# Kernel optimization log

Hardware: AMD Instinct MI355X
Metric: run time of the kernel (lower is better)

Reference implementation:

```python
import jax, jax.numpy as jnp
import numpy as np


def _dequantize_int4(qweight, scales, qzeros, blocksize):
    """Unpack int4 weights (two nibbles per byte along N) and dequantize.

    qweight: [K, N/2] int (byte values 0..255); low nibble = even col, high nibble = odd col
    scales:  [groups, N] float32, groups = K // blocksize
    qzeros:  [groups, N/2] int (packed like qweight)
    returns: [K, N] float32 dequantized weight, w = (q - z) * s per group along K
    """
    K, Nh = qweight.shape
    N = Nh * 2
    groups = scales.shape[0]
    low = (qweight & 0xF).astype(jnp.float32)
    high = ((qweight >> 4) & 0xF).astype(jnp.float32)
    wq = jnp.stack([low, high], axis=-1).reshape(K, N)  # [K, N]
    zl = (qzeros & 0xF).astype(jnp.float32)
    zh = ((qzeros >> 4) & 0xF).astype(jnp.float32)
    zq = jnp.stack([zl, zh], axis=-1).reshape(groups, N)  # [groups, N]
    # group-wise dequant along K without materializing repeated scale/zero tables
    w = (wq.reshape(groups, blocksize, N) - zq[:, None, :]) * scales[:, None, :]
    return w.reshape(K, N)


def setup_inputs() -> dict:
    key = jax.random.key(0)
    k1, k2, k3, k4, k5 = jax.random.split(key, 5)
    B, S, K = 32, 64, 4096
    N_PAD = 32064
    BLOCKSIZE = 128
    GROUPS = K // BLOCKSIZE
    x = jax.random.normal(k1, (B, S, K), dtype=jnp.float32)
    qweight = jax.random.randint(k2, (K, N_PAD // 2), 0, 256, dtype=jnp.int32)
    scales = jax.random.uniform(k3, (GROUPS, N_PAD), dtype=jnp.float32) * 0.02 + 1e-3
    qzeros = jax.random.randint(k4, (GROUPS, N_PAD // 2), 0, 256, dtype=jnp.int32)
    bias = jax.random.normal(k5, (N_PAD,), dtype=jnp.float32) * 0.01
    return {"x": x, "qweight": qweight, "scales": scales, "qzeros": qzeros,
            "bias": bias, "blocksize": BLOCKSIZE, "n_dim": 32000}


def reference(x, qweight, scales, qzeros, bias, blocksize, n_dim):
    # mimic module.forward with acc_test=False: keep only the last token
    if x.ndim > 3:
        x = x.reshape(-1, x.shape[-2], x.shape[-1])
    x_last = x[:, -1:, :]  # [B, 1, K]
    w = _dequantize_int4(qweight, scales, qzeros, blocksize)  # [K, N_pad]
    out = jnp.einsum('bsk,kn->bsn', x_last, w) + bias  # mm_bias_int4
    return out[:, :, :n_dim]  # strip vocab padding
```

## Files before the change

kernel.cpp:

```cpp
#include <hip/hip_runtime.h>
#include <hip/hip_bf16.h>


typedef _Float16 f16x8 __attribute__((ext_vector_type(8)));
typedef _Float16 f16x2 __attribute__((ext_vector_type(2)));
typedef float f32x4 __attribute__((ext_vector_type(4)));
typedef int i32x2 __attribute__((ext_vector_type(2)));

#define K_DIM 4096
#define NP 16032
#define NSC 32064
#define NOUT 32000
#define S_LEN 64
#define QROWB ((size_t)NP * 4)
#define QSTEP (32u * (uint32_t)NP * 4u)

__global__ void prep_a_kernel(const float* __restrict__ x,
                              _Float16* __restrict__ aws) {
    int tid = blockIdx.x * 256 + threadIdx.x;
    int m = tid >> 9;
    int q = tid & 511;
    const float* xp = x + ((size_t)m * S_LEN + (S_LEN - 1)) * K_DIM + q * 8;
    f32x4 u0 = *(const f32x4*)xp;
    f32x4 u1 = *(const f32x4*)(xp + 4);
    int ks = q >> 2;
    int h = q & 3;
    int mblk = m >> 4;
    f16x8 d;
#pragma unroll
    for (int j = 0; j < 4; ++j) {
        d[j] = (_Float16)u0[j];
        d[4 + j] = (_Float16)u1[j];
    }
    *(f16x8*)(aws + ((size_t)((ks * 2 + mblk) * 64 + h * 16 + (m & 15))) * 8) = d;
}

__global__ __launch_bounds__(512, 4)
void q4gemm_kernel(const int* __restrict__ qw,
                   const float* __restrict__ scales,
                   const int* __restrict__ qzeros,
                   const float* __restrict__ bias,
                   const _Float16* __restrict__ aws,
                   float* __restrict__ out) {
    __shared__ float red[8 * 2048];

    const int tid = threadIdx.x;
    const int w = tid >> 6;
    const int l = tid & 63;
    const int h = l >> 4;
    const int c = l & 15;
    const int n0 = blockIdx.x * 64;
    const int np0 = n0 >> 1;

    const char* qwb = (const char*)qw;
    uint32_t qoff = (uint32_t)((w * 512 + 8 * h) * (size_t)NP + np0 + 2 * c) * 4u;

    f32x4 acc0[4] = {};
    f32x4 acc1[4] = {};
    f16x2 vz[4], vs[4];
    f32x4 gsc;
    i32x2 gzw;
    i32x2 qa[8], qb[8];
    f16x8 afa0, afa1, afb0, afb1;

#define QLD(buf)                                                              \
    do {                                                                      \
        _Pragma("unroll") for (int j = 0; j < 8; ++j)                         \
            buf[j] = *(const i32x2*)(qwb + qoff + (size_t)j * QROWB);         \
        qoff += QSTEP;                                                        \
    } while (0)

#define GRP_LOAD(g)                                                           \
    do {                                                                      \
        int gg = (g) > 31 ? 31 : (g);                                         \
        gsc = *(const f32x4*)(scales + (size_t)gg * NSC + n0 + 4 * c);        \
        gzw = *(const i32x2*)(qzeros + (size_t)gg * NP + np0 + 2 * c);        \
    } while (0)

#define GRP_EXPAND()                                                          \
    do {                                                                      \
        _Pragma("unroll") for (int s = 0; s < 4; ++s) {                       \
            const int bs = s >> 1, o = s & 1;                                 \
            int zn = (gzw[bs] >> (4 * o)) & 15;                               \
            int z16 = 0x6400 | (o ? (zn << 4) : zn);                          \
            int zp = z16 | (z16 << 16);                                       \
            vz[s] = __builtin_bit_cast(f16x2, zp);                            \
            float sf = gsc[s] * (o ? 0.0625f : 1.0f);                         \
            _Float16 hf = (_Float16)sf;                                       \
            f16x2 sp = {hf, hf};                                              \
            vs[s] = sp;                                                       \
        }                                                                     \
    } while (0)

#define ALD(A0, A1, tloc)                                                     \
    do {                                                                      \
        int ksg_ = w * 16 + (tloc);                                           \
        A0 = *(const f16x8*)(aws + ((size_t)(ksg_ * 2 + 0) * 64 + l) * 8);    \
        A1 = *(const f16x8*)(aws + ((size_t)(ksg_ * 2 + 1) * 64 + l) * 8);    \
    } while (0)

#define COMPUTE(buf, A0, A1)                                                  \
    do {                                                                      \
        _Pragma("unroll") for (int bs = 0; bs < 2; ++bs) {                    \
            int tc[4];                                                        \
            _Pragma("unroll") for (int p = 0; p < 4; ++p)                     \
                tc[p] = (buf[2 * p + 1][bs] << 16) | buf[2 * p][bs];          \
            _Pragma("unroll") for (int o = 0; o < 2; ++o) {                   \
                const int s = 2 * bs + o;                                     \
                const int msk = o ? 0x00F000F0 : 0x000F000F;                  \
                int4 bi;                                                      \
                _Pragma("unroll") for (int p = 0; p < 4; ++p) {               \
                    int vqi = (tc[p] & msk) | 0x64006400;                     \
                    f16x2 vq = __builtin_bit_cast(f16x2, vqi);                \
                    f16x2 r = (vq - vz[s]) * vs[s];                           \
                    bi[p] = __builtin_bit_cast(int, r);                       \
                }                                                             \
                f16x8 b = __builtin_bit_cast(f16x8, bi);                      \
                acc0[s] = __builtin_amdgcn_mfma_f32_16x16x32_f16(A0, b, acc0[s], 0, 0, 0); \
                acc1[s] = __builtin_amdgcn_mfma_f32_16x16x32_f16(A1, b, acc1[s], 0, 0, 0); \
            }                                                                 \
        }                                                                     \
    } while (0)

    QLD(qa);
    GRP_LOAD(w * 4);
    GRP_EXPAND();
    GRP_LOAD(w * 4 + 1);
    ALD(afa0, afa1, 0);

#pragma unroll
    for (int tt = 0; tt < 8; ++tt) {
        QLD(qb);
        ALD(afb0, afb1, 2 * tt + 1);
        if (tt != 0 && (tt & 1) == 0) {
            GRP_EXPAND();
            GRP_LOAD(w * 4 + tt / 2 + 1);
        }
        COMPUTE(qa, afa0, afa1);
        if (tt < 7) {
            QLD(qa);
            ALD(afa0, afa1, 2 * tt + 2);
        }
        COMPUTE(qb, afb0, afb1);
    }

#pragma unroll
    for (int s = 0; s < 4; ++s)
#pragma unroll
        for (int r = 0; r < 4; ++r) {
            red[w * 2048 + (h * 4 + r) * 64 + 4 * c + s] = acc0[s][r];
            red[w * 2048 + (16 + h * 4 + r) * 64 + 4 * c + s] = acc1[s][r];
        }

    __syncthreads();

#pragma unroll
    for (int i = 0; i < 4; ++i) {
        int e = i * 512 + tid;
        float sum = 0.f;
#pragma unroll
        for (int ww = 0; ww < 8; ++ww) sum += red[ww * 2048 + e];
        int m = e >> 6;
        int n = n0 + (e & 63);
        out[(size_t)m * NOUT + n] = sum + bias[n];
    }
}

extern "C" void kernel_launch(void* const* d_in, const int* in_sizes, int n_in,
                              void* d_out, int out_size, void* d_ws, size_t ws_size,
                              hipStream_t stream) {
    const float* x       = (const float*)d_in[0];
    const int*   qweight = (const int*)d_in[1];
    const float* scales  = (const float*)d_in[2];
    const int*   qzeros  = (const int*)d_in[3];
    const float* bias    = (const float*)d_in[4];

    _Float16* aws = (_Float16*)d_ws;
    float* out = (float*)d_out;

    prep_a_kernel<<<64, 256, 0, stream>>>(x, aws);
    q4gemm_kernel<<<500, 512, 0, stream>>>(qweight, scales, qzeros, bias, aws, out);
}
```

Baseline: 50.47 us.

## Widen GEMM tile to 128 columns per block with 16-byte weight loads

Each block now covers 128 output columns instead of 64. Each lane loads 16-byte qweight/qzeros vectors and handles 8 column subsets, which doubles the accumulators per thread. The cross-wave reduction is split into two passes through the same shared buffer, one for each M half, with an extra barrier between them. This halves the grid to 250 blocks and lowers the occupancy hint to 2 blocks per CU, trading parallelism and register pressure for wider memory transactions and less per-block overhead.

```diff
diff --git a/kernel.cpp b/kernel.cpp
--- a/kernel.cpp
+++ b/kernel.cpp
@@ -6,6 +6,7 @@
 typedef _Float16 f16x2 __attribute__((ext_vector_type(2)));
 typedef float f32x4 __attribute__((ext_vector_type(4)));
 typedef int i32x2 __attribute__((ext_vector_type(2)));
+typedef int i32x4 __attribute__((ext_vector_type(4)));
 
 #define K_DIM 4096
 #define NP 16032
@@ -35,7 +36,7 @@
     *(f16x8*)(aws + ((size_t)((ks * 2 + mblk) * 64 + h * 16 + (m & 15))) * 8) = d;
 }
 
-__global__ __launch_bounds__(512, 4)
+__global__ __launch_bounds__(512, 2)
 void q4gemm_kernel(const int* __restrict__ qw,
                    const float* __restrict__ scales,
                    const int* __restrict__ qzeros,
@@ -49,43 +50,45 @@
     const int l = tid & 63;
     const int h = l >> 4;
     const int c = l & 15;
-    const int n0 = blockIdx.x * 64;
+    const int n0 = blockIdx.x * 128;
     const int np0 = n0 >> 1;
 
     const char* qwb = (const char*)qw;
-    uint32_t qoff = (uint32_t)((w * 512 + 8 * h) * (size_t)NP + np0 + 2 * c) * 4u;
-
-    f32x4 acc0[4] = {};
-    f32x4 acc1[4] = {};
-    f16x2 vz[4], vs[4];
-    f32x4 gsc;
-    i32x2 gzw;
-    i32x2 qa[8], qb[8];
+    uint32_t qoff = (uint32_t)((w * 512 + 8 * h) * (size_t)NP + np0 + 4 * c) * 4u;
+
+    f32x4 acc0[8] = {};
+    f32x4 acc1[8] = {};
+    f16x2 vz[8], vs[8];
+    f32x4 gsc0, gsc1;
+    i32x4 gzw;
+    i32x4 qa[8], qb[8];
     f16x8 afa0, afa1, afb0, afb1;
 
 #define QLD(buf)                                                              \
     do {                                                                      \
         _Pragma("unroll") for (int j = 0; j < 8; ++j)                         \
-            buf[j] = *(const i32x2*)(qwb + qoff + (size_t)j * QROWB);         \
+            buf[j] = *(const i32x4*)(qwb + qoff + (size_t)j * QROWB);         \
         qoff += QSTEP;                                                        \
     } while (0)
 
 #define GRP_LOAD(g)                                                           \
     do {                                                                      \
         int gg = (g) > 31 ? 31 : (g);                                         \
-        gsc = *(const f32x4*)(scales + (size_t)gg * NSC + n0 + 4 * c);        \
-        gzw = *(const i32x2*)(qzeros + (size_t)gg * NP + np0 + 2 * c);        \
+        gsc0 = *(const f32x4*)(scales + (size_t)gg * NSC + n0 + 8 * c);       \
+        gsc1 = *(const f32x4*)(scales + (size_t)gg * NSC + n0 + 8 * c + 4);   \
+        gzw = *(const i32x4*)(qzeros + (size_t)gg * NP + np0 + 4 * c);        \
     } while (0)
 
 #define GRP_EXPAND()                                                          \
     do {                                                                      \
-        _Pragma("unroll") for (int s = 0; s < 4; ++s) {                       \
-            const int bs = s >> 1, o = s & 1;                                 \
-            int zn = (gzw[bs] >> (4 * o)) & 15;                               \
+        _Pragma("unroll") for (int s = 0; s < 8; ++s) {                       \
+            const int q = s >> 1, o = s & 1;                                  \
+            int zn = (gzw[q] >> (4 * o)) & 15;                                \
             int z16 = 0x6400 | (o ? (zn << 4) : zn);                          \
             int zp = z16 | (z16 << 16);                                       \
             vz[s] = __builtin_bit_cast(f16x2, zp);                            \
-            float sf = gsc[s] * (o ? 0.0625f : 1.0f);                         \
+            float sraw = (s < 4) ? gsc0[s] : gsc1[s - 4];                     \
+            float sf = sraw * (o ? 0.0625f : 1.0f);                           \
             _Float16 hf = (_Float16)sf;                                       \
             f16x2 sp = {hf, hf};                                              \
             vs[s] = sp;                                                       \
@@ -101,12 +104,12 @@
 
 #define COMPUTE(buf, A0, A1)                                                  \
     do {                                                                      \
-        _Pragma("unroll") for (int bs = 0; bs < 2; ++bs) {                    \
+        _Pragma("unroll") for (int q = 0; q < 4; ++q) {                       \
             int tc[4];                                                        \
             _Pragma("unroll") for (int p = 0; p < 4; ++p)                     \
-                tc[p] = (buf[2 * p + 1][bs] << 16) | buf[2 * p][bs];          \
+                tc[p] = (buf[2 * p + 1][q] << 16) | buf[2 * p][q];            \
             _Pragma("unroll") for (int o = 0; o < 2; ++o) {                   \
-                const int s = 2 * bs + o;                                     \
+                const int s = 2 * q + o;                                      \
                 const int msk = o ? 0x00F000F0 : 0x000F000F;                  \
                 int4 bi;                                                      \
                 _Pragma("unroll") for (int p = 0; p < 4; ++p) {               \
@@ -144,25 +147,42 @@
         COMPUTE(qb, afb0, afb1);
     }
 
-#pragma unroll
-    for (int s = 0; s < 4; ++s)
-#pragma unroll
-        for (int r = 0; r < 4; ++r) {
-            red[w * 2048 + (h * 4 + r) * 64 + 4 * c + s] = acc0[s][r];
-            red[w * 2048 + (16 + h * 4 + r) * 64 + 4 * c + s] = acc1[s][r];
-        }
-
+    float bv[4];
+
+#pragma unroll
+    for (int s = 0; s < 8; ++s)
+#pragma unroll
+        for (int r = 0; r < 4; ++r)
+            red[w * 2048 + (h * 4 + r) * 128 + 8 * c + s] = acc0[s][r];
     __syncthreads();
-
 #pragma unroll
     for (int i = 0; i < 4; ++i) {
         int e = i * 512 + tid;
         float sum = 0.f;
 #pragma unroll
         for (int ww = 0; ww < 8; ++ww) sum += red[ww * 2048 + e];
-        int m = e >> 6;
-        int n = n0 + (e & 63);
-        out[(size_t)m * NOUT + n] = sum + bias[n];
+        int m = e >> 7;
+        int n = n0 + (e & 127);
+        bv[i] = bias[n];
+        out[(size_t)m * NOUT + n] = sum + bv[i];
+    }
+    __syncthreads();
+
+#pragma unroll
+    for (int s = 0; s < 8; ++s)
+#pragma unroll
+        for (int r = 0; r < 4; ++r)
+            red[w * 2048 + (h * 4 + r) * 128 + 8 * c + s] = acc1[s][r];
+    __syncthreads();
+#pragma unroll
+    for (int i = 0; i < 4; ++i) {
+        int e = i * 512 + tid;
+        float sum = 0.f;
+#pragma unroll
+        for (int ww = 0; ww < 8; ++ww) sum += red[ww * 2048 + e];
+        int m = 16 + (e >> 7);
+        int n = n0 + (e & 127);
+        out[(size_t)m * NOUT + n] = sum + bv[i];
     }
 }
 
@@ -179,5 +199,5 @@
     float* out = (float*)d_out;
 
     prep_a_kernel<<<64, 256, 0, stream>>>(x, aws);
-    q4gemm_kernel<<<500, 512, 0, stream>>>(qweight, scales, qzeros, bias, aws, out);
+    q4gemm_kernel<<<250, 512, 0, stream>>>(qweight, scales, qzeros, bias, aws, out);
 }
```

Result: no change. 50.85 us (+0.7%).
